# Performance work log

Hardware: AMD Instinct MI355X
Metric: run time of the kernel (lower is better)

## Reference

```python
import jax, jax.numpy as jnp
import numpy as np
import math

N_HEADS = 8

def setup_inputs() -> dict:
    key = jax.random.key(0)
    qkv = jax.random.normal(key, (4, 1536, 2048), dtype=jnp.float32)
    return {"qkv": qkv}

def reference(qkv) -> jnp.ndarray:
    bs, width, length = qkv.shape
    assert width % (3 * N_HEADS) == 0
    ch = width // (3 * N_HEADS)
    q, k, v = jnp.split(qkv, 3, axis=1)  # each [bs, n_heads*ch, length]
    scale = 1.0 / math.sqrt(math.sqrt(ch))
    q = (q * scale).reshape(bs * N_HEADS, ch, length)
    k = (k * scale).reshape(bs * N_HEADS, ch, length)
    v = v.reshape(bs * N_HEADS, ch, length)
    # scores: [B*H, t, s]
    weight = jnp.einsum('bct,bcs->bts', q, k)
    weight = jax.nn.softmax(weight, axis=-1)
    a = jnp.einsum('bts,bcs->bct', weight, v)  # [B*H, ch, length]
    return a.reshape(bs, -1, length)
```

## Files before the change

### kernel.cpp

```cpp
#include <hip/hip_runtime.h>
#include <hip/hip_bf16.h>

typedef unsigned short u16;
typedef unsigned int u32;
typedef __attribute__((ext_vector_type(8))) short short8;
typedef __attribute__((ext_vector_type(16))) float f32x16;

#define SEQ 2048

__device__ __forceinline__ u16 f2bf(float f) {
  union { __hip_bfloat16 h; u16 u; } c;
  c.h = __float2bfloat16(f);
  return c.u;
}

__device__ __forceinline__ float exp2fast(float x) {
  return __builtin_amdgcn_exp2f(x);
}

__global__ __launch_bounds__(256) void prep_all(const float* __restrict__ qkv,
                                                u16* __restrict__ wsQ,
                                                u16* __restrict__ wsK,
                                                u16* __restrict__ wsV) {
  const int tid = threadIdx.x;
  const int bh = blockIdx.y;
  const int b = bh >> 3, h = bh & 7;
  const int z = blockIdx.z;

  if (z == 2) {
#pragma unroll
    for (int rep = 0; rep < 2; ++rep) {
      const int il = rep * 256 + tid;
      const int j = 2 * blockIdx.x + (il >> 8);
      const int slot = il & 255;
      const int lane = slot & 63;
      const int ctks = slot >> 6;
      const int ct = ctks >> 1, ks2 = ctks & 1;
      const int hi = lane >> 5, tl = lane & 31;
      const int cc = ct * 32 + tl;
      const int s = j * 32 + ks2 * 16 + hi * 8;
      const float* src = qkv + ((size_t)b * 1536 + 1024 + (size_t)h * 64 + cc) * SEQ + s;
      const float4 v0 = *(const float4*)(src);
      const float4 v1 = *(const float4*)(src + 4);
      union { u16 us[8]; uint4 q; } pk;
      pk.us[0] = f2bf(v0.x); pk.us[1] = f2bf(v0.y); pk.us[2] = f2bf(v0.z); pk.us[3] = f2bf(v0.w);
      pk.us[4] = f2bf(v1.x); pk.us[5] = f2bf(v1.y); pk.us[6] = f2bf(v1.z); pk.us[7] = f2bf(v1.w);
      *(uint4*)(wsV + ((size_t)bh * 16384 + (size_t)j * 256 + slot) * 8) = pk.q;
    }
    return;
  }

  __shared__ float tile[64 * 67];
  const int t0 = blockIdx.x * 64;
  const int isK = z;
  const float scale = 0.42466090014692505f;
  const size_t inbase = ((size_t)b * 1536 + (size_t)isK * 512 + (size_t)h * 64) * SEQ;

  const int c = tid >> 2, tq = tid & 3;
#pragma unroll
  for (int u = 0; u < 4; ++u) {
    const int t = tq * 16 + u * 4;
    const float4 v = *(const float4*)(qkv + inbase + (size_t)c * SEQ + t0 + t);
    tile[c * 67 + t + 0] = v.x * scale;
    tile[c * 67 + t + 1] = v.y * scale;
    tile[c * 67 + t + 2] = v.z * scale;
    tile[c * 67 + t + 3] = v.w * scale;
  }
  __syncthreads();
  const int tt = tid >> 2, cq = tid & 3, c0 = cq * 16;
  u16* dst = (isK ? wsK : wsQ) + ((size_t)bh * SEQ + t0 + tt) * 64 + c0;
  union { u16 us[8]; uint4 v; } p0, p1;
#pragma unroll
  for (int i = 0; i < 8; ++i) p0.us[i] = f2bf(tile[(c0 + i) * 67 + tt]);
#pragma unroll
  for (int i = 0; i < 8; ++i) p1.us[i] = f2bf(tile[(c0 + 8 + i) * 67 + tt]);
  *(uint4*)(dst) = p0.v;
  *(uint4*)(dst + 8) = p1.v;
}

__global__ __launch_bounds__(512) void attn_kernel(const u16* __restrict__ wsQ,
                                                   const u16* __restrict__ wsK,
                                                   const u16* __restrict__ wsV,
                                                   float* __restrict__ out) {
  __shared__ __align__(16) char smem[65536];
  __shared__ float Xl[4][2][32];

  const int tid = threadIdx.x;
  const int w = tid >> 6;
  const int lane = tid & 63;
  const int tl = lane & 31;
  const int hi = lane >> 5;
  const int sh = w >> 2;
  const int u = w & 3;
  const int ts = tid & 255;

  const int bid = blockIdx.x;
  const int vb = (bid & 7) * 32 + (bid >> 3);
  const int tblk = vb & 7, bh = vb >> 3;
  const int tq0 = tblk * 256 + u * 64;

  const u16* qb = wsQ + (size_t)bh * (SEQ * 64);
  const u16* kb = wsK + (size_t)bh * (SEQ * 64);
  const u16* vstream = wsV + (size_t)bh * 131072 + lane * 8;

  char* Kbuf = smem + sh * 16384;

  short8 qf[2][4];
#pragma unroll
  for (int cb = 0; cb < 2; ++cb) {
    const u16* qrow = qb + (size_t)(tq0 + cb * 32 + tl) * 64 + 8 * hi;
#pragma unroll
    for (int ks = 0; ks < 4; ++ks) qf[cb][ks] = *(const short8*)(qrow + 16 * ks);
  }

  f32x16 acc[4];
#pragma unroll
  for (int a = 0; a < 4; ++a)
#pragma unroll
    for (int r = 0; r < 16; ++r) acc[a][r] = 0.0f;
  float la0[2] = {0, 0};
  float la1[2] = {0, 0};

  uint4 kg[2];

#define STAGE_LOAD(S)                                                       \
  do {                                                                      \
    _Pragma("unroll")                                                       \
    for (int _it = 0; _it < 2; ++_it) {                                     \
      const int _idx = _it * 256 + ts;                                      \
      const int _row = _idx >> 3, _g = _idx & 7;                            \
      kg[_it] = *(const uint4*)(kb + (size_t)((S) + _row) * 64 + _g * 8);   \
    }                                                                       \
  } while (0)

#define STAGE_WRITE(PBUF)                                                   \
  do {                                                                      \
    char* _kd = Kbuf + (PBUF) * 8192;                                       \
    _Pragma("unroll")                                                       \
    for (int _it = 0; _it < 2; ++_it) {                                     \
      const int _idx = _it * 256 + ts;                                      \
      const int _row = _idx >> 3, _g = _idx & 7;                            \
      *(uint4*)(_kd + _row * 128 + ((_g ^ (_row & 7)) << 4)) = kg[_it];     \
    }                                                                       \
  } while (0)

#define PACK_P(PV16, PF0, PF1)                                                        \
  do {                                                                                \
    u32 _pk[8];                                                                       \
    _Pragma("unroll")                                                                 \
    for (int _q = 0; _q < 8; ++_q) {                                                  \
      const float _lo = PV16[2 * _q], _hi = PV16[2 * _q + 1];                         \
      asm("v_cvt_pk_bf16_f32 %0, %1, %2" : "=v"(_pk[_q]) : "v"(_lo), "v"(_hi));       \
    }                                                                                 \
    asm("v_permlane32_swap_b32 %0, %1" : "+v"(_pk[0]), "+v"(_pk[2]));                 \
    asm("v_permlane32_swap_b32 %0, %1" : "+v"(_pk[1]), "+v"(_pk[3]));                 \
    asm("v_permlane32_swap_b32 %0, %1" : "+v"(_pk[4]), "+v"(_pk[6]));                 \
    asm("v_permlane32_swap_b32 %0, %1" : "+v"(_pk[5]), "+v"(_pk[7]));                 \
    union { u32 u[4]; short8 v; } _f0, _f1;                                           \
    _f0.u[0] = _pk[0]; _f0.u[1] = _pk[1]; _f0.u[2] = _pk[2]; _f0.u[3] = _pk[3];       \
    _f1.u[0] = _pk[4]; _f1.u[1] = _pk[5]; _f1.u[2] = _pk[6]; _f1.u[3] = _pk[7];       \
    PF0 = _f0.v; PF1 = _f1.v;                                                         \
  } while (0)

#define SUBTILE(SS, JJ)                                                               \
  do {                                                                                \
    const int krow = (SS) * 32 + tl;                                                  \
    short8 kf[4];                                                                     \
    _Pragma("unroll")                                                                 \
    for (int ks = 0; ks < 4; ++ks)                                                    \
      kf[ks] = *(const short8*)(Ks + krow * 128 + (((2 * ks + hi) ^ (krow & 7)) << 4)); \
    f32x16 s0 = {0, 0, 0, 0, 0, 0, 0, 0, 0, 0, 0, 0, 0, 0, 0, 0};                    \
    f32x16 s1 = s0;                                                                   \
    __builtin_amdgcn_s_setprio(1);                                                    \
    _Pragma("unroll")                                                                 \
    for (int ks = 0; ks < 4; ++ks) {                                                  \
      s0 = __builtin_amdgcn_mfma_f32_32x32x16_bf16(kf[ks], qf[0][ks], s0, 0, 0, 0);   \
      s1 = __builtin_amdgcn_mfma_f32_32x32x16_bf16(kf[ks], qf[1][ks], s1, 0, 0, 0);   \
    }                                                                                 \
    __builtin_amdgcn_s_setprio(0);                                                    \
    const u16* vp = vstream + (size_t)(JJ) * 2048;                                    \
    const short8 vf0 = *(const short8*)(vp);                                          \
    const short8 vf1 = *(const short8*)(vp + 512);                                    \
    const short8 vf2 = *(const short8*)(vp + 1024);                                   \
    const short8 vf3 = *(const short8*)(vp + 1536);                                   \
    _Pragma("unroll")                                                                 \
    for (int r = 0; r < 16; ++r) s0[r] = exp2fast(s0[r]);                             \
    _Pragma("unroll")                                                                 \
    for (int r = 0; r < 16; ++r) s1[r] = exp2fast(s1[r]);                             \
    _Pragma("unroll")                                                                 \
    for (int j = 0; j < 2; ++j) {                                                     \
      la0[j] += ((s0[8 * j] + s0[8 * j + 1]) + (s0[8 * j + 2] + s0[8 * j + 3])) +     \
                ((s0[8 * j + 4] + s0[8 * j + 5]) + (s0[8 * j + 6] + s0[8 * j + 7]));  \
      la1[j] += ((s1[8 * j] + s1[8 * j + 1]) + (s1[8 * j + 2] + s1[8 * j + 3])) +     \
                ((s1[8 * j + 4] + s1[8 * j + 5]) + (s1[8 * j + 6] + s1[8 * j + 7]));  \
    }                                                                                 \
    short8 pf00, pf01, pf10, pf11;                                                    \
    PACK_P(s0, pf00, pf01);                                                           \
    PACK_P(s1, pf10, pf11);                                                           \
    __builtin_amdgcn_s_setprio(1);                                                    \
    acc[0] = __builtin_amdgcn_mfma_f32_32x32x16_bf16(vf0, pf00, acc[0], 0, 0, 0);     \
    acc[0] = __builtin_amdgcn_mfma_f32_32x32x16_bf16(vf1, pf01, acc[0], 0, 0, 0);     \
    acc[1] = __builtin_amdgcn_mfma_f32_32x32x16_bf16(vf2, pf00, acc[1], 0, 0, 0);     \
    acc[1] = __builtin_amdgcn_mfma_f32_32x32x16_bf16(vf3, pf01, acc[1], 0, 0, 0);     \
    acc[2] = __builtin_amdgcn_mfma_f32_32x32x16_bf16(vf0, pf10, acc[2], 0, 0, 0);     \
    acc[2] = __builtin_amdgcn_mfma_f32_32x32x16_bf16(vf1, pf11, acc[2], 0, 0, 0);     \
    acc[3] = __builtin_amdgcn_mfma_f32_32x32x16_bf16(vf2, pf10, acc[3], 0, 0, 0);     \
    acc[3] = __builtin_amdgcn_mfma_f32_32x32x16_bf16(vf3, pf11, acc[3], 0, 0, 0);     \
    __builtin_amdgcn_s_setprio(0);                                                    \
  } while (0)

  STAGE_LOAD(sh * 1024);
  STAGE_WRITE(0);
  __syncthreads();

  for (int i = 0; i < 16; ++i) {
    if (i < 15) STAGE_LOAD(sh * 1024 + (i + 1) * 64);

    const char* Ks = Kbuf + (i & 1) * 8192;
    const int jbase = sh * 32 + i * 2;

    SUBTILE(0, jbase);
    if (i < 15) STAGE_WRITE((i + 1) & 1);
    SUBTILE(1, jbase + 1);

    __syncthreads();
  }

  float l0 = la0[0] + la0[1];
  float l1 = la1[0] + la1[1];
  l0 += __shfl_xor(l0, 32, 64);
  l1 += __shfl_xor(l1, 32, 64);

  float* Xa = (float*)smem + u * 4096;
  if (sh == 1) {
#pragma unroll
    for (int a = 0; a < 4; ++a)
#pragma unroll
      for (int r = 0; r < 16; ++r) Xa[(a * 16 + r) * 64 + lane] = acc[a][r];
    Xl[u][0][tl] = l0;
    Xl[u][1][tl] = l1;
  }
  __syncthreads();
  if (sh == 0) {
    float* ob = out + (size_t)bh * 64 * SEQ;
    const float inv0 = 1.0f / (l0 + Xl[u][0][tl]);
    const float inv1 = 1.0f / (l1 + Xl[u][1][tl]);
#pragma unroll
    for (int r = 0; r < 16; ++r) {
      const int c0 = (r & 3) + 8 * (r >> 2) + 4 * hi;
      const int ta = tq0 + tl, tb2 = tq0 + 32 + tl;
      ob[(size_t)c0 * SEQ + ta] = (acc[0][r] + Xa[(0 * 16 + r) * 64 + lane]) * inv0;
      ob[(size_t)(c0 + 32) * SEQ + ta] = (acc[1][r] + Xa[(1 * 16 + r) * 64 + lane]) * inv0;
      ob[(size_t)c0 * SEQ + tb2] = (acc[2][r] + Xa[(2 * 16 + r) * 64 + lane]) * inv1;
      ob[(size_t)(c0 + 32) * SEQ + tb2] = (acc[3][r] + Xa[(3 * 16 + r) * 64 + lane]) * inv1;
    }
  }
}

extern "C" void kernel_launch(void* const* d_in, const int* in_sizes, int n_in,
                              void* d_out, int out_size, void* d_ws, size_t ws_size,
                              hipStream_t stream) {
  const float* qkv = (const float*)d_in[0];
  float* out = (float*)d_out;
  u16* wsQ = (u16*)d_ws;
  u16* wsK = wsQ + (size_t)32 * SEQ * 64;
  u16* wsV = wsK + (size_t)32 * SEQ * 64;

  prep_all<<<dim3(32, 32, 3), 256, 0, stream>>>(qkv, wsQ, wsK, wsV);
  attn_kernel<<<256, 512, 0, stream>>>(wsQ, wsK, wsV, out);
}
```

Before: 55.68 us.

## Software-pipeline QK MFMA of next subtile with softmax/PV of current

Splits the per-subtile work into a QK score step and a finish step (exp, row sums, pack, PV MMA). The loop now computes the next subtile's scores before finishing the current one, and issues the next iteration's first QK right after the barrier. The goal is to let matrix-core work overlap the exp and pack ALU work and hide LDS latency. In exchange it keeps two more score accumulators live, which raises register pressure, and it adds an extra barrier after the loop.

```diff
diff --git a/kernel.cpp b/kernel.cpp
--- a/kernel.cpp
+++ b/kernel.cpp
@@ -162,70 +162,80 @@
     PF0 = _f0.v; PF1 = _f1.v;                                                         \
   } while (0)
 
-#define SUBTILE(SS, JJ)                                                               \
-  do {                                                                                \
-    const int krow = (SS) * 32 + tl;                                                  \
-    short8 kf[4];                                                                     \
-    _Pragma("unroll")                                                                 \
-    for (int ks = 0; ks < 4; ++ks)                                                    \
-      kf[ks] = *(const short8*)(Ks + krow * 128 + (((2 * ks + hi) ^ (krow & 7)) << 4)); \
-    f32x16 s0 = {0, 0, 0, 0, 0, 0, 0, 0, 0, 0, 0, 0, 0, 0, 0, 0};                    \
-    f32x16 s1 = s0;                                                                   \
-    __builtin_amdgcn_s_setprio(1);                                                    \
-    _Pragma("unroll")                                                                 \
-    for (int ks = 0; ks < 4; ++ks) {                                                  \
-      s0 = __builtin_amdgcn_mfma_f32_32x32x16_bf16(kf[ks], qf[0][ks], s0, 0, 0, 0);   \
-      s1 = __builtin_amdgcn_mfma_f32_32x32x16_bf16(kf[ks], qf[1][ks], s1, 0, 0, 0);   \
-    }                                                                                 \
-    __builtin_amdgcn_s_setprio(0);                                                    \
-    const u16* vp = vstream + (size_t)(JJ) * 2048;                                    \
-    const short8 vf0 = *(const short8*)(vp);                                          \
-    const short8 vf1 = *(const short8*)(vp + 512);                                    \
-    const short8 vf2 = *(const short8*)(vp + 1024);                                   \
-    const short8 vf3 = *(const short8*)(vp + 1536);                                   \
-    _Pragma("unroll")                                                                 \
-    for (int r = 0; r < 16; ++r) s0[r] = exp2fast(s0[r]);                             \
-    _Pragma("unroll")                                                                 \
-    for (int r = 0; r < 16; ++r) s1[r] = exp2fast(s1[r]);                             \
-    _Pragma("unroll")                                                                 \
-    for (int j = 0; j < 2; ++j) {                                                     \
-      la0[j] += ((s0[8 * j] + s0[8 * j + 1]) + (s0[8 * j + 2] + s0[8 * j + 3])) +     \
-                ((s0[8 * j + 4] + s0[8 * j + 5]) + (s0[8 * j + 6] + s0[8 * j + 7]));  \
-      la1[j] += ((s1[8 * j] + s1[8 * j + 1]) + (s1[8 * j + 2] + s1[8 * j + 3])) +     \
-                ((s1[8 * j + 4] + s1[8 * j + 5]) + (s1[8 * j + 6] + s1[8 * j + 7]));  \
-    }                                                                                 \
-    short8 pf00, pf01, pf10, pf11;                                                    \
-    PACK_P(s0, pf00, pf01);                                                           \
-    PACK_P(s1, pf10, pf11);                                                           \
-    __builtin_amdgcn_s_setprio(1);                                                    \
-    acc[0] = __builtin_amdgcn_mfma_f32_32x32x16_bf16(vf0, pf00, acc[0], 0, 0, 0);     \
-    acc[0] = __builtin_amdgcn_mfma_f32_32x32x16_bf16(vf1, pf01, acc[0], 0, 0, 0);     \
-    acc[1] = __builtin_amdgcn_mfma_f32_32x32x16_bf16(vf2, pf00, acc[1], 0, 0, 0);     \
-    acc[1] = __builtin_amdgcn_mfma_f32_32x32x16_bf16(vf3, pf01, acc[1], 0, 0, 0);     \
-    acc[2] = __builtin_amdgcn_mfma_f32_32x32x16_bf16(vf0, pf10, acc[2], 0, 0, 0);     \
-    acc[2] = __builtin_amdgcn_mfma_f32_32x32x16_bf16(vf1, pf11, acc[2], 0, 0, 0);     \
-    acc[3] = __builtin_amdgcn_mfma_f32_32x32x16_bf16(vf2, pf10, acc[3], 0, 0, 0);     \
-    acc[3] = __builtin_amdgcn_mfma_f32_32x32x16_bf16(vf3, pf11, acc[3], 0, 0, 0);     \
-    __builtin_amdgcn_s_setprio(0);                                                    \
+#define QKSTEP(SS, BUF, S0, S1)                                                         \
+  do {                                                                                  \
+    const char* _Ks = Kbuf + (BUF) * 8192;                                              \
+    const int _krow = (SS) * 32 + tl;                                                   \
+    short8 _kf[4];                                                                      \
+    _Pragma("unroll")                                                                   \
+    for (int _ks = 0; _ks < 4; ++_ks)                                                   \
+      _kf[_ks] = *(const short8*)(_Ks + _krow * 128 + (((2 * _ks + hi) ^ (_krow & 7)) << 4)); \
+    _Pragma("unroll")                                                                   \
+    for (int _r = 0; _r < 16; ++_r) { S0[_r] = 0.0f; S1[_r] = 0.0f; }                   \
+    __builtin_amdgcn_s_setprio(1);                                                      \
+    _Pragma("unroll")                                                                   \
+    for (int _ks = 0; _ks < 4; ++_ks) {                                                 \
+      S0 = __builtin_amdgcn_mfma_f32_32x32x16_bf16(_kf[_ks], qf[0][_ks], S0, 0, 0, 0);  \
+      S1 = __builtin_amdgcn_mfma_f32_32x32x16_bf16(_kf[_ks], qf[1][_ks], S1, 0, 0, 0);  \
+    }                                                                                   \
+    __builtin_amdgcn_s_setprio(0);                                                      \
+  } while (0)
+
+#define FINISH(S0, S1, JJ)                                                              \
+  do {                                                                                  \
+    const u16* _vp = vstream + (size_t)(JJ) * 2048;                                     \
+    const short8 _vf0 = *(const short8*)(_vp);                                          \
+    const short8 _vf1 = *(const short8*)(_vp + 512);                                    \
+    const short8 _vf2 = *(const short8*)(_vp + 1024);                                   \
+    const short8 _vf3 = *(const short8*)(_vp + 1536);                                   \
+    _Pragma("unroll")                                                                   \
+    for (int _r = 0; _r < 16; ++_r) S0[_r] = exp2fast(S0[_r]);                          \
+    _Pragma("unroll")                                                                   \
+    for (int _r = 0; _r < 16; ++_r) S1[_r] = exp2fast(S1[_r]);                          \
+    _Pragma("unroll")                                                                   \
+    for (int _j = 0; _j < 2; ++_j) {                                                    \
+      la0[_j] += ((S0[8 * _j] + S0[8 * _j + 1]) + (S0[8 * _j + 2] + S0[8 * _j + 3])) + \
+                 ((S0[8 * _j + 4] + S0[8 * _j + 5]) + (S0[8 * _j + 6] + S0[8 * _j + 7])); \
+      la1[_j] += ((S1[8 * _j] + S1[8 * _j + 1]) + (S1[8 * _j + 2] + S1[8 * _j + 3])) + \
+                 ((S1[8 * _j + 4] + S1[8 * _j + 5]) + (S1[8 * _j + 6] + S1[8 * _j + 7])); \
+    }                                                                                   \
+    short8 _pf00, _pf01, _pf10, _pf11;                                                  \
+    PACK_P(S0, _pf00, _pf01);                                                           \
+    PACK_P(S1, _pf10, _pf11);                                                           \
+    __builtin_amdgcn_s_setprio(1);                                                      \
+    acc[0] = __builtin_amdgcn_mfma_f32_32x32x16_bf16(_vf0, _pf00, acc[0], 0, 0, 0);     \
+    acc[0] = __builtin_amdgcn_mfma_f32_32x32x16_bf16(_vf1, _pf01, acc[0], 0, 0, 0);     \
+    acc[1] = __builtin_amdgcn_mfma_f32_32x32x16_bf16(_vf2, _pf00, acc[1], 0, 0, 0);     \
+    acc[1] = __builtin_amdgcn_mfma_f32_32x32x16_bf16(_vf3, _pf01, acc[1], 0, 0, 0);     \
+    acc[2] = __builtin_amdgcn_mfma_f32_32x32x16_bf16(_vf0, _pf10, acc[2], 0, 0, 0);     \
+    acc[2] = __builtin_amdgcn_mfma_f32_32x32x16_bf16(_vf1, _pf11, acc[2], 0, 0, 0);     \
+    acc[3] = __builtin_amdgcn_mfma_f32_32x32x16_bf16(_vf2, _pf10, acc[3], 0, 0, 0);     \
+    acc[3] = __builtin_amdgcn_mfma_f32_32x32x16_bf16(_vf3, _pf11, acc[3], 0, 0, 0);     \
+    __builtin_amdgcn_s_setprio(0);                                                      \
   } while (0)
 
   STAGE_LOAD(sh * 1024);
   STAGE_WRITE(0);
   __syncthreads();
 
+  f32x16 sA0, sA1, sB0, sB1;
+  QKSTEP(0, 0, sA0, sA1);
+
   for (int i = 0; i < 16; ++i) {
     if (i < 15) STAGE_LOAD(sh * 1024 + (i + 1) * 64);
-
-    const char* Ks = Kbuf + (i & 1) * 8192;
     const int jbase = sh * 32 + i * 2;
 
-    SUBTILE(0, jbase);
+    QKSTEP(1, i & 1, sB0, sB1);
+    FINISH(sA0, sA1, jbase);
+
     if (i < 15) STAGE_WRITE((i + 1) & 1);
-    SUBTILE(1, jbase + 1);
-
     __syncthreads();
-  }
-
+
+    if (i < 15) QKSTEP(0, (i + 1) & 1, sA0, sA1);
+    FINISH(sB0, sB1, jbase + 1);
+  }
+
+  __syncthreads();
   float l0 = la0[0] + la0[1];
   float l1 = la1[0] + la1[1];
   l0 += __shfl_xor(l0, 32, 64);
```

Result: slower. 57.07 us (+2.5%).
